# Optimization experiments

Measured on AMD Instinct MI355X. Metric: run time of the kernel, lower is better.

Reference implementation:

```python
import jax, jax.numpy as jnp
import numpy as np


def setup_inputs() -> dict:
    key = jax.random.key(0)
    k1, k2 = jax.random.split(key)
    x = jax.random.normal(k1, (16, 4096, 256), dtype=jnp.float32)
    embedding = jax.random.normal(k2, (1024, 256), dtype=jnp.float32)
    return {"x": x, "embedding": embedding}


def reference(x, embedding):
    # which_dim = -1 (default): no permute.
    shape = x.shape
    xf = x.reshape(-1, shape[-1])  # [N, D]
    x_sq = jnp.sum(xf * xf, axis=-1, keepdims=True)          # [N, 1]
    e_sq = jnp.sum(embedding * embedding, axis=-1)           # [K]
    dist = -(x_sq - 2.0 * (xf @ embedding.T) + e_sq[None, :])  # [N, K]
    embed_indices = jnp.argmax(dist, axis=1)                 # [N]
    embed_indices = embed_indices.reshape(shape[:-1])        # [B, S]
    quantization = embedding[embed_indices]                  # [B, S, D]
    return (quantization, embed_indices)
```

## Files before the change

kernel.cpp:

```cpp
#include <hip/hip_runtime.h>
#include <hip/hip_fp16.h>
#include <math.h>

#define MROWS   65536
#define NCODES  1024
#define KD      256
#define MARGIN  0.25f

typedef unsigned short u16;
typedef __attribute__((ext_vector_type(8))) _Float16 hfrag;
typedef __attribute__((ext_vector_type(4))) float f32x4;

#define IOFF ((size_t)MROWS * KD)

__device__ __forceinline__ float addrn(float a, float b) {
    float d; asm("v_add_f32 %0, %1, %2" : "=v"(d) : "v"(a), "v"(b)); return d;
}

__device__ __forceinline__ float sumsq_vf8ic4(const float* __restrict__ xr) {
    float a[4][8];
#pragma unroll
    for (int i = 0; i < 4; ++i)
#pragma unroll
        for (int l = 0; l < 8; ++l) a[i][l] = 0.f;
#pragma unroll
    for (int m = 0; m < 8; ++m)
#pragma unroll
        for (int i = 0; i < 4; ++i)
#pragma unroll
            for (int l = 0; l < 8; ++l) {
                float v = xr[m * 32 + i * 8 + l];
                a[i][l] = fmaf(v, v, a[i][l]);
            }
    float cc[8];
#pragma unroll
    for (int l = 0; l < 8; ++l)
        cc[l] = addrn(addrn(addrn(a[0][l], a[1][l]), a[2][l]), a[3][l]);
    float u0 = addrn(cc[0], cc[4]), u1 = addrn(cc[1], cc[5]);
    float u2 = addrn(cc[2], cc[6]), u3 = addrn(cc[3], cc[7]);
    return addrn(addrn(u0, u2), addrn(u1, u3));
}

__global__ __launch_bounds__(256)
void vq_pack(const float* __restrict__ src, u16* __restrict__ dh,
             unsigned int* __restrict__ cnt) {
    if (cnt && blockIdx.x == 0 && threadIdx.x == 0) *cnt = 0;
    __shared__ __align__(16) float lx[16 * 260];
    const int t = threadIdx.x;
    const size_t base = (size_t)blockIdx.x * 16 * 256;
#pragma unroll
    for (int qq = 0; qq < 4; ++qq) {
        int i4 = qq * 256 + t;
        int row = i4 >> 6, col = (i4 & 63) * 4;
        *(float4*)(lx + row * 260 + col) = *(const float4*)(src + base + (size_t)i4 * 4);
    }
    __syncthreads();
#pragma unroll
    for (int i = 0; i < 2; ++i) {
        int s = t + 256 * i;
        int kb = s >> 6, lane = s & 63;
        int r = lane & 15, kg = lane >> 4;
        int k0 = kb * 32 + kg * 8;
        u16 vh[8];
#pragma unroll
        for (int j = 0; j < 8; ++j) {
            float v = lx[r * 260 + k0 + j];
            vh[j] = __half_as_ushort(__float2half(v));
        }
        size_t off = (((size_t)blockIdx.x * 8 + kb) * 64 + lane) * 8;
        *(ulonglong2*)(dh + off) = *(ulonglong2*)vh;
    }
}

__global__ __launch_bounds__(256)
void vq_sumsq_llvm(const float* __restrict__ src, float* __restrict__ out) {
    __shared__ float lx[64 * 257];
    const int t = threadIdx.x;
    const size_t base = (size_t)blockIdx.x * 64 * 256;
#pragma unroll
    for (int qq = 0; qq < 16; ++qq) {
        int idx4 = qq * 256 + t;
        int row = idx4 >> 6, col4 = idx4 & 63;
        *(float4*)(lx + row * 257 + col4 * 4) = *(const float4*)(src + base + (size_t)idx4 * 4);
    }
    __syncthreads();
    if (t < 64) out[blockIdx.x * 64 + t] = sumsq_vf8ic4(lx + t * 257);
}

__global__ __launch_bounds__(256)
void vq_transpose(const float* __restrict__ emb, float* __restrict__ embT) {
    __shared__ float ld[64][65];
    const int t = threadIdx.x;
    const int c0 = blockIdx.x * 64, k0 = blockIdx.y * 64;
#pragma unroll
    for (int u = 0; u < 16; ++u) {
        int i = u * 256 + t;
        int r = i >> 6, col = i & 63;
        ld[r][col] = emb[(size_t)(c0 + r) * 256 + k0 + col];
    }
    __syncthreads();
#pragma unroll
    for (int u = 0; u < 16; ++u) {
        int i = u * 256 + t;
        int r = i >> 6, col = i & 63;
        embT[(size_t)(k0 + r) * 1024 + c0 + col] = ld[col][r];
    }
}

__global__ __launch_bounds__(256, 2)
void vq_gemm(const u16* __restrict__ Ah, const u16* __restrict__ Eh,
             const float* __restrict__ esq, float* __restrict__ tw) {
    extern __shared__ u16 ldsA[];
    const int t = threadIdx.x;
    const int wave = t >> 6, lane = t & 63;
    const int wm = wave >> 1, wn = wave & 1;
    const int q = lane >> 4, c = lane & 15;
    const int m0 = blockIdx.x * 128;
    const int mrb8 = blockIdx.x * 64;

#pragma unroll
    for (int u = 0; u < 16; ++u) {
        int f = wave * 16 + u;
        const u16* srcp = Ah + ((size_t)(mrb8 + f) * 64 + lane) * 8;
        __builtin_amdgcn_global_load_lds((const unsigned int*)srcp,
                                         (unsigned int*)(ldsA + f * 512), 16, 0, 0);
    }
    __syncthreads();

    auto LOADB = [&](int s, hfrag* dst) {
        const int f0 = ((s >> 3) * 64) + (wn * 4) * 8 + (s & 7);
#pragma unroll
        for (int ni = 0; ni < 4; ++ni)
            dst[ni] = *(const hfrag*)(Eh + (size_t)(f0 + ni * 8) * 512 + lane * 8);
    };
    auto LDA = [&](int s, hfrag* dst) {
        const int ks = s & 7;
#pragma unroll
        for (int mi = 0; mi < 4; ++mi)
            dst[mi] = *(const hfrag*)(ldsA + ((wm * 4 + mi) * 8 + ks) * 512 + lane * 8);
    };

    float b1[16], s2v[16], bi[16];
#pragma unroll
    for (int r = 0; r < 16; ++r) { b1[r] = INFINITY; s2v[r] = INFINITY; bi[r] = 0.f; }

    f32x4 acc[4][4];
#pragma unroll
    for (int mi = 0; mi < 4; ++mi)
#pragma unroll
        for (int ni = 0; ni < 4; ++ni) acc[mi][ni] = 0.f;

    hfrag bA[4], bB[4];
    LOADB(0, bA);
    LOADB(1, bB);

    for (int sp = 0; sp < 32; ++sp) {
        const int s0 = sp * 2, s1 = sp * 2 + 1;
        {
            hfrag nx[4];
            LOADB(s0 + 2 < 64 ? s0 + 2 : 0, nx);
            hfrag af[4];
            LDA(s0, af);
#pragma unroll
            for (int mi = 0; mi < 4; ++mi)
#pragma unroll
                for (int ni = 0; ni < 4; ++ni)
                    acc[mi][ni] = __builtin_amdgcn_mfma_f32_16x16x32_f16(af[mi], bA[ni], acc[mi][ni], 0, 0, 0);
#pragma unroll
            for (int ni = 0; ni < 4; ++ni) bA[ni] = nx[ni];
        }
        {
            hfrag nx[4];
            LOADB(s1 + 2 < 64 ? s1 + 2 : 0, nx);
            hfrag af[4];
            LDA(s1, af);
#pragma unroll
            for (int mi = 0; mi < 4; ++mi)
#pragma unroll
                for (int ni = 0; ni < 4; ++ni)
                    acc[mi][ni] = __builtin_amdgcn_mfma_f32_16x16x32_f16(af[mi], bB[ni], acc[mi][ni], 0, 0, 0);
#pragma unroll
            for (int ni = 0; ni < 4; ++ni) bB[ni] = nx[ni];
        }
        if ((s1 & 7) == 7) {
            const int nqi = s1 >> 3;
#pragma unroll
            for (int ni = 0; ni < 4; ++ni) {
                const int code = nqi * 128 + wn * 64 + ni * 16 + c;
                const float e2 = esq[code];
                const float ci = (float)code;
#pragma unroll
                for (int mi = 0; mi < 4; ++mi)
#pragma unroll
                    for (int j = 0; j < 4; ++j) {
                        const int r = mi * 4 + j;
                        float sc = fmaf(-2.f, acc[mi][ni][j], e2);
                        bool lt = sc < b1[r];
                        s2v[r] = fminf(s2v[r], lt ? b1[r] : sc);
                        if (lt) { b1[r] = sc; bi[r] = ci; }
                    }
            }
#pragma unroll
            for (int mi = 0; mi < 4; ++mi)
#pragma unroll
                for (int ni = 0; ni < 4; ++ni) acc[mi][ni] = 0.f;
        }
    }

#pragma unroll
    for (int r = 0; r < 16; ++r) {
#pragma unroll
        for (int mm = 1; mm < 16; mm <<= 1) {
            float ob = __shfl_xor(b1[r], mm, 64);
            float os = __shfl_xor(s2v[r], mm, 64);
            float oi = __shfl_xor(bi[r], mm, 64);
            if (ob < b1[r]) { s2v[r] = fminf(b1[r], os); b1[r] = ob; bi[r] = oi; }
            else            { s2v[r] = fminf(s2v[r], ob); }
        }
    }
    if (c == 0) {
#pragma unroll
        for (int mi = 0; mi < 4; ++mi)
#pragma unroll
            for (int j = 0; j < 4; ++j) {
                int row = m0 + wm * 64 + mi * 16 + q * 4 + j;
                size_t o = (size_t)row * 8 + wn * 4;
                int r = mi * 4 + j;
                tw[o + 0] = b1[r];
                tw[o + 1] = s2v[r];
                tw[o + 2] = bi[r];
            }
    }
}

__global__ void vq_reduce2(const float* __restrict__ tw, float* __restrict__ idxf,
                           unsigned int* __restrict__ cnt, int* __restrict__ list) {
    int row = blockIdx.x * 256 + threadIdx.x;
    float b0 = tw[(size_t)row * 8 + 0], s0 = tw[(size_t)row * 8 + 1], i0 = tw[(size_t)row * 8 + 2];
    float b1 = tw[(size_t)row * 8 + 4], s1 = tw[(size_t)row * 8 + 5], i1 = tw[(size_t)row * 8 + 6];
    float b, s2, bidx;
    if (b0 <= b1) { b = b0; bidx = i0; s2 = fminf(s0, b1); }
    else          { b = b1; bidx = i1; s2 = fminf(s1, b0); }
    idxf[row] = bidx;
    if (s2 - b < MARGIN) {
        unsigned int pos = atomicAdd(cnt, 1u);
        list[pos] = row;
    }
}

__global__ __launch_bounds__(256)
void vq_refine1(const float* __restrict__ x, const float* __restrict__ embT,
                const float* __restrict__ esq, const int* __restrict__ list,
                const unsigned int* __restrict__ cnt, float* __restrict__ idxf) {
    __shared__ __align__(16) float xs[8][260];
    __shared__ float xsq_s[8];
    __shared__ float lb[8][4];
    __shared__ int   li[8][4];
    const int t = threadIdx.x;
    const int wave = t >> 6, lane = t & 63;
    const unsigned int n = *cnt;
    float e2q[4];
#pragma unroll
    for (int qq = 0; qq < 4; ++qq) e2q[qq] = esq[qq * 256 + t];

    for (unsigned int g = blockIdx.x; g * 8u < n; g += gridDim.x) {
        const unsigned int r0 = g * 8u;
        const int nr = (int)min(8u, n - r0);
        __syncthreads();
#pragma unroll
        for (int u = 0; u < 2; ++u) {
            int s = u * 256 + t;
            int rr = s >> 6, l4 = s & 63;
            if (rr < nr) {
                int row = list[r0 + rr];
                *(float4*)(&xs[rr][l4 * 4]) = *(const float4*)(x + (size_t)row * 256 + l4 * 4);
            }
        }
        __syncthreads();
        if (t < nr) xsq_s[t] = sumsq_vf8ic4(&xs[t][0]);
        __syncthreads();

        float d[8][4];
#pragma unroll
        for (int r = 0; r < 8; ++r)
#pragma unroll
            for (int qq = 0; qq < 4; ++qq) d[r][qq] = 0.f;

        for (int kq = 0; kq < 64; ++kq) {
            float ev[4][4];
#pragma unroll
            for (int j = 0; j < 4; ++j)
#pragma unroll
                for (int qq = 0; qq < 4; ++qq)
                    ev[qq][j] = embT[(size_t)(kq * 4 + j) * 1024 + qq * 256 + t];
            float4 xf[8];
#pragma unroll
            for (int r = 0; r < 8; ++r) xf[r] = *(const float4*)(&xs[r][kq * 4]);
#pragma unroll
            for (int r = 0; r < 8; ++r)
#pragma unroll
                for (int qq = 0; qq < 4; ++qq) {
                    d[r][qq] = fmaf(xf[r].x, ev[qq][0], d[r][qq]);
                    d[r][qq] = fmaf(xf[r].y, ev[qq][1], d[r][qq]);
                    d[r][qq] = fmaf(xf[r].z, ev[qq][2], d[r][qq]);
                    d[r][qq] = fmaf(xf[r].w, ev[qq][3], d[r][qq]);
                }
        }
#pragma unroll
        for (int r = 0; r < 8; ++r) {
            float sv = INFINITY; int bc = 0x7fffffff;
#pragma unroll
            for (int qq = 0; qq < 4; ++qq) {
                float s = addrn(fmaf(-2.f, d[r][qq], xsq_s[r]), e2q[qq]);
                if (s < sv) { sv = s; bc = qq * 256 + t; }
            }
#pragma unroll
            for (int mm = 1; mm < 64; mm <<= 1) {
                float ob = __shfl_xor(sv, mm, 64);
                int oi = __shfl_xor(bc, mm, 64);
                if (ob < sv || (ob == sv && oi < bc)) { sv = ob; bc = oi; }
            }
            if (lane == 0) { lb[r][wave] = sv; li[r][wave] = bc; }
        }
        __syncthreads();
        if (t < nr) {
            float best = lb[t][0]; int bix = li[t][0];
#pragma unroll
            for (int w = 1; w < 4; ++w) {
                float ob = lb[t][w]; int oi = li[t][w];
                if (ob < best || (ob == best && oi < bix)) { best = ob; bix = oi; }
            }
            idxf[list[r0 + t]] = (float)bix;
        }
    }
}

__global__ void vq_gather(const float* __restrict__ emb, const float* __restrict__ idx_f,
                          float* __restrict__ qout) {
    int row = blockIdx.x * 4 + (threadIdx.x >> 6);
    int l = threadIdx.x & 63;
    int idx = (int)idx_f[row];
    float4 v = *(const float4*)(emb + (size_t)idx * KD + l * 4);
    *(float4*)(qout + (size_t)row * KD + l * 4) = v;
}

extern "C" void kernel_launch(void* const* d_in, const int* in_sizes, int n_in,
                              void* d_out, int out_size, void* d_ws, size_t ws_size,
                              hipStream_t stream) {
    const float* x   = (const float*)d_in[0];
    const float* emb = (const float*)d_in[1];
    float* out  = (float*)d_out;
    float* idxf = out + IOFF;

    u16* Ah = (u16*)out;
    float* embT = (float*)((char*)d_out + (32u << 20));

    char* ws = (char*)d_ws;
    u16* Eh    = (u16*)(ws);
    float* esq = (float*)(ws + (512 << 10));
    float* tw  = (float*)(ws + (1 << 20));
    unsigned int* cnt = (unsigned int*)(ws + ((size_t)3 << 20) + (512 << 10));
    int* list = (int*)(ws + ((size_t)3 << 20) + (512 << 10) + 256);

    vq_pack<<<dim3(MROWS / 16), dim3(256), 0, stream>>>(x, Ah, cnt);
    vq_pack<<<dim3(NCODES / 16), dim3(256), 0, stream>>>(emb, Eh, nullptr);
    vq_sumsq_llvm<<<dim3(NCODES / 64), dim3(256), 0, stream>>>(emb, esq);
    vq_transpose<<<dim3(16, 4), dim3(256), 0, stream>>>(emb, embT);
    vq_gemm<<<dim3(MROWS / 128), dim3(256), 65536, stream>>>(Ah, Eh, esq, tw);
    vq_reduce2<<<dim3(MROWS / 256), dim3(256), 0, stream>>>(tw, idxf, cnt, list);
    vq_refine1<<<dim3(512), dim3(256), 0, stream>>>(x, embT, esq, list, cnt, idxf);
    vq_gather<<<dim3(MROWS / 4), dim3(256), 0, stream>>>(emb, idxf, out);
}
```

Baseline: 138.8 us.

## Fuse embedding prep, in-block reduction and gather; widen GEMM to eight waves

Merges the three embedding preprocessing kernels (fp16 pack, squared norms, transpose) into one kernel that loads each tile once. The GEMM now runs 512 threads with a four-way code split, so each block covers 256 codes per pass in half as many steps. The per-row best and second-best across waves are combined in LDS, which removes the separate reduce kernel. The index write, flagging of ambiguous rows and quantization gather are fused into one kernel, and the refine kernel rewrites the gathered rows for the rows it fixes. This cuts launches and global round trips, but the launch bound of 512 threads with 4 blocks may squeeze registers and cause spills in the MFMA loop.

```diff
diff --git a/kernel.cpp b/kernel.cpp
--- a/kernel.cpp
+++ b/kernel.cpp
@@ -44,7 +44,7 @@
 __global__ __launch_bounds__(256)
 void vq_pack(const float* __restrict__ src, u16* __restrict__ dh,
              unsigned int* __restrict__ cnt) {
-    if (cnt && blockIdx.x == 0 && threadIdx.x == 0) *cnt = 0;
+    if (blockIdx.x == 0 && threadIdx.x == 0) *cnt = 0;
     __shared__ __align__(16) float lx[16 * 260];
     const int t = threadIdx.x;
     const size_t base = (size_t)blockIdx.x * 16 * 256;
@@ -73,54 +73,55 @@
 }
 
 __global__ __launch_bounds__(256)
-void vq_sumsq_llvm(const float* __restrict__ src, float* __restrict__ out) {
+void vq_prep_emb(const float* __restrict__ emb, u16* __restrict__ Eh,
+                 float* __restrict__ esq, float* __restrict__ embT) {
     __shared__ float lx[64 * 257];
     const int t = threadIdx.x;
-    const size_t base = (size_t)blockIdx.x * 64 * 256;
+    const int c0 = blockIdx.x * 64;
+    const size_t base = (size_t)c0 * 256;
 #pragma unroll
     for (int qq = 0; qq < 16; ++qq) {
         int idx4 = qq * 256 + t;
         int row = idx4 >> 6, col4 = idx4 & 63;
-        *(float4*)(lx + row * 257 + col4 * 4) = *(const float4*)(src + base + (size_t)idx4 * 4);
-    }
-    __syncthreads();
-    if (t < 64) out[blockIdx.x * 64 + t] = sumsq_vf8ic4(lx + t * 257);
-}
-
-__global__ __launch_bounds__(256)
-void vq_transpose(const float* __restrict__ emb, float* __restrict__ embT) {
-    __shared__ float ld[64][65];
-    const int t = threadIdx.x;
-    const int c0 = blockIdx.x * 64, k0 = blockIdx.y * 64;
-#pragma unroll
-    for (int u = 0; u < 16; ++u) {
-        int i = u * 256 + t;
-        int r = i >> 6, col = i & 63;
-        ld[r][col] = emb[(size_t)(c0 + r) * 256 + k0 + col];
-    }
-    __syncthreads();
-#pragma unroll
-    for (int u = 0; u < 16; ++u) {
-        int i = u * 256 + t;
-        int r = i >> 6, col = i & 63;
-        embT[(size_t)(k0 + r) * 1024 + c0 + col] = ld[col][r];
-    }
-}
-
-__global__ __launch_bounds__(256, 2)
+        *(float4*)(lx + row * 257 + col4 * 4) = *(const float4*)(emb + base + (size_t)idx4 * 4);
+    }
+    __syncthreads();
+    if (t < 64) esq[c0 + t] = sumsq_vf8ic4(lx + t * 257);
+#pragma unroll
+    for (int i = 0; i < 8; ++i) {
+        int s = i * 256 + t;
+        int fl = s >> 6, lane = s & 63;
+        int rb_l = fl >> 3, kb = fl & 7;
+        int r = rb_l * 16 + (lane & 15), kg = lane >> 4;
+        int k0 = kb * 32 + kg * 8;
+        u16 vh[8];
+#pragma unroll
+        for (int j = 0; j < 8; ++j)
+            vh[j] = __half_as_ushort(__float2half(lx[r * 257 + k0 + j]));
+        size_t off = (((size_t)(blockIdx.x * 4 + rb_l) * 8 + kb) * 64 + lane) * 8;
+        *(ulonglong2*)(Eh + off) = *(ulonglong2*)vh;
+    }
+#pragma unroll
+    for (int i = 0; i < 64; ++i) {
+        int k = i * 4 + (t >> 6), col = t & 63;
+        embT[(size_t)k * 1024 + c0 + col] = lx[col * 257 + k];
+    }
+}
+
+__global__ __launch_bounds__(512, 4)
 void vq_gemm(const u16* __restrict__ Ah, const u16* __restrict__ Eh,
              const float* __restrict__ esq, float* __restrict__ tw) {
     extern __shared__ u16 ldsA[];
     const int t = threadIdx.x;
     const int wave = t >> 6, lane = t & 63;
-    const int wm = wave >> 1, wn = wave & 1;
+    const int wm = wave >> 2, wn = wave & 3;
     const int q = lane >> 4, c = lane & 15;
     const int m0 = blockIdx.x * 128;
     const int mrb8 = blockIdx.x * 64;
 
 #pragma unroll
-    for (int u = 0; u < 16; ++u) {
-        int f = wave * 16 + u;
+    for (int u = 0; u < 8; ++u) {
+        int f = wave * 8 + u;
         const u16* srcp = Ah + ((size_t)(mrb8 + f) * 64 + lane) * 8;
         __builtin_amdgcn_global_load_lds((const unsigned int*)srcp,
                                          (unsigned int*)(ldsA + f * 512), 16, 0, 0);
@@ -128,7 +129,7 @@
     __syncthreads();
 
     auto LOADB = [&](int s, hfrag* dst) {
-        const int f0 = ((s >> 3) * 64) + (wn * 4) * 8 + (s & 7);
+        const int f0 = (s >> 3) * 128 + (wn * 4) * 8 + (s & 7);
 #pragma unroll
         for (int ni = 0; ni < 4; ++ni)
             dst[ni] = *(const hfrag*)(Eh + (size_t)(f0 + ni * 8) * 512 + lane * 8);
@@ -154,11 +155,11 @@
     LOADB(0, bA);
     LOADB(1, bB);
 
-    for (int sp = 0; sp < 32; ++sp) {
+    for (int sp = 0; sp < 16; ++sp) {
         const int s0 = sp * 2, s1 = sp * 2 + 1;
         {
             hfrag nx[4];
-            LOADB(s0 + 2 < 64 ? s0 + 2 : 0, nx);
+            LOADB(s0 + 2 < 32 ? s0 + 2 : 0, nx);
             hfrag af[4];
             LDA(s0, af);
 #pragma unroll
@@ -171,7 +172,7 @@
         }
         {
             hfrag nx[4];
-            LOADB(s1 + 2 < 64 ? s1 + 2 : 0, nx);
+            LOADB(s1 + 2 < 32 ? s1 + 2 : 0, nx);
             hfrag af[4];
             LDA(s1, af);
 #pragma unroll
@@ -183,10 +184,10 @@
             for (int ni = 0; ni < 4; ++ni) bB[ni] = nx[ni];
         }
         if ((s1 & 7) == 7) {
-            const int nqi = s1 >> 3;
+            const int p = s1 >> 3;
 #pragma unroll
             for (int ni = 0; ni < 4; ++ni) {
-                const int code = nqi * 128 + wn * 64 + ni * 16 + c;
+                const int code = p * 256 + wn * 64 + ni * 16 + c;
                 const float e2 = esq[code];
                 const float ci = (float)code;
 #pragma unroll
@@ -218,44 +219,78 @@
             else            { s2v[r] = fminf(s2v[r], ob); }
         }
     }
+    __syncthreads();
+    float* sm = (float*)ldsA;
     if (c == 0) {
 #pragma unroll
         for (int mi = 0; mi < 4; ++mi)
 #pragma unroll
             for (int j = 0; j < 4; ++j) {
-                int row = m0 + wm * 64 + mi * 16 + q * 4 + j;
-                size_t o = (size_t)row * 8 + wn * 4;
                 int r = mi * 4 + j;
-                tw[o + 0] = b1[r];
-                tw[o + 1] = s2v[r];
-                tw[o + 2] = bi[r];
-            }
-    }
-}
-
-__global__ void vq_reduce2(const float* __restrict__ tw, float* __restrict__ idxf,
-                           unsigned int* __restrict__ cnt, int* __restrict__ list) {
-    int row = blockIdx.x * 256 + threadIdx.x;
-    float b0 = tw[(size_t)row * 8 + 0], s0 = tw[(size_t)row * 8 + 1], i0 = tw[(size_t)row * 8 + 2];
-    float b1 = tw[(size_t)row * 8 + 4], s1 = tw[(size_t)row * 8 + 5], i1 = tw[(size_t)row * 8 + 6];
-    float b, s2, bidx;
-    if (b0 <= b1) { b = b0; bidx = i0; s2 = fminf(s0, b1); }
-    else          { b = b1; bidx = i1; s2 = fminf(s1, b0); }
-    idxf[row] = bidx;
-    if (s2 - b < MARGIN) {
-        unsigned int pos = atomicAdd(cnt, 1u);
-        list[pos] = row;
+                int row_l = wm * 64 + mi * 16 + q * 4 + j;
+                sm[row_l * 12 + wn * 3 + 0] = b1[r];
+                sm[row_l * 12 + wn * 3 + 1] = s2v[r];
+                sm[row_l * 12 + wn * 3 + 2] = bi[r];
+            }
+    }
+    __syncthreads();
+    if (t < 128) {
+        float b = INFINITY, s2 = INFINITY, bidx = 0.f;
+#pragma unroll
+        for (int w = 0; w < 4; ++w) {
+            float ob = sm[t * 12 + w * 3 + 0];
+            float os = sm[t * 12 + w * 3 + 1];
+            float oi = sm[t * 12 + w * 3 + 2];
+            if (ob < b) { s2 = fminf(b, os); b = ob; bidx = oi; }
+            else        { s2 = fminf(s2, ob); }
+        }
+        size_t row = (size_t)(m0 + t);
+        tw[row * 4 + 0] = b;
+        tw[row * 4 + 1] = s2;
+        tw[row * 4 + 2] = bidx;
     }
 }
 
 __global__ __launch_bounds__(256)
-void vq_refine1(const float* __restrict__ x, const float* __restrict__ embT,
-                const float* __restrict__ esq, const int* __restrict__ list,
-                const unsigned int* __restrict__ cnt, float* __restrict__ idxf) {
+void vq_flag_gather(const float* __restrict__ tw, const float* __restrict__ emb,
+                    float* __restrict__ idxf, float* __restrict__ quant,
+                    unsigned int* __restrict__ cnt, int* __restrict__ list) {
+    __shared__ int idx_l[64];
+    const int t = threadIdx.x;
+    const int r0 = blockIdx.x * 64;
+    if (t < 64) {
+        int row = r0 + t;
+        float b  = tw[(size_t)row * 4 + 0];
+        float s2 = tw[(size_t)row * 4 + 1];
+        int bidx = (int)tw[(size_t)row * 4 + 2];
+        idxf[row] = (float)bidx;
+        idx_l[t] = bidx;
+        if (s2 - b < MARGIN) {
+            unsigned int pos = atomicAdd(cnt, 1u);
+            list[pos] = row;
+        }
+    }
+    __syncthreads();
+    const int lane = t & 63, w = t >> 6;
+#pragma unroll
+    for (int u = 0; u < 16; ++u) {
+        int rl = u * 4 + w;
+        int idx = idx_l[rl];
+        *(float4*)(quant + (size_t)(r0 + rl) * 256 + lane * 4) =
+            *(const float4*)(emb + (size_t)idx * 256 + lane * 4);
+    }
+}
+
+__global__ __launch_bounds__(256)
+void vq_refine1(const float* __restrict__ x, const float* __restrict__ emb,
+                const float* __restrict__ embT, const float* __restrict__ esq,
+                const int* __restrict__ list, const unsigned int* __restrict__ cnt,
+                float* __restrict__ idxf, float* __restrict__ quant) {
     __shared__ __align__(16) float xs[8][260];
     __shared__ float xsq_s[8];
     __shared__ float lb[8][4];
     __shared__ int   li[8][4];
+    __shared__ int   li2[8];
     const int t = threadIdx.x;
     const int wave = t >> 6, lane = t & 63;
     const unsigned int n = *cnt;
@@ -331,17 +366,20 @@
                 if (ob < best || (ob == best && oi < bix)) { best = ob; bix = oi; }
             }
             idxf[list[r0 + t]] = (float)bix;
-        }
-    }
-}
-
-__global__ void vq_gather(const float* __restrict__ emb, const float* __restrict__ idx_f,
-                          float* __restrict__ qout) {
-    int row = blockIdx.x * 4 + (threadIdx.x >> 6);
-    int l = threadIdx.x & 63;
-    int idx = (int)idx_f[row];
-    float4 v = *(const float4*)(emb + (size_t)idx * KD + l * 4);
-    *(float4*)(qout + (size_t)row * KD + l * 4) = v;
+            li2[t] = bix;
+        }
+        __syncthreads();
+#pragma unroll
+        for (int rr = 0; rr < 2; ++rr) {
+            int rl = wave * 2 + rr;
+            if (rl < nr) {
+                int row = list[r0 + rl];
+                int idx = li2[rl];
+                *(float4*)(quant + (size_t)row * 256 + lane * 4) =
+                    *(const float4*)(emb + (size_t)idx * 256 + lane * 4);
+            }
+        }
+    }
 }
 
 extern "C" void kernel_launch(void* const* d_in, const int* in_sizes, int n_in,
@@ -353,21 +391,18 @@
     float* idxf = out + IOFF;
 
     u16* Ah = (u16*)out;
-    float* embT = (float*)((char*)d_out + (32u << 20));
 
     char* ws = (char*)d_ws;
     u16* Eh    = (u16*)(ws);
     float* esq = (float*)(ws + (512 << 10));
-    float* tw  = (float*)(ws + (1 << 20));
-    unsigned int* cnt = (unsigned int*)(ws + ((size_t)3 << 20) + (512 << 10));
-    int* list = (int*)(ws + ((size_t)3 << 20) + (512 << 10) + 256);
+    unsigned int* cnt = (unsigned int*)(ws + (640 << 10));
+    int* list  = (int*)(ws + (640 << 10) + 256);
+    float* embT = (float*)(ws + (1 << 20));
+    float* tw   = (float*)(ws + (2 << 20));
 
     vq_pack<<<dim3(MROWS / 16), dim3(256), 0, stream>>>(x, Ah, cnt);
-    vq_pack<<<dim3(NCODES / 16), dim3(256), 0, stream>>>(emb, Eh, nullptr);
-    vq_sumsq_llvm<<<dim3(NCODES / 64), dim3(256), 0, stream>>>(emb, esq);
-    vq_transpose<<<dim3(16, 4), dim3(256), 0, stream>>>(emb, embT);
-    vq_gemm<<<dim3(MROWS / 128), dim3(256), 65536, stream>>>(Ah, Eh, esq, tw);
-    vq_reduce2<<<dim3(MROWS / 256), dim3(256), 0, stream>>>(tw, idxf, cnt, list);
-    vq_refine1<<<dim3(512), dim3(256), 0, stream>>>(x, embT, esq, list, cnt, idxf);
-    vq_gather<<<dim3(MROWS / 4), dim3(256), 0, stream>>>(emb, idxf, out);
-}
+    vq_prep_emb<<<dim3(16), dim3(256), 0, stream>>>(emb, Eh, esq, embT);
+    vq_gemm<<<dim3(MROWS / 128), dim3(512), 65536, stream>>>(Ah, Eh, esq, tw);
+    vq_flag_gather<<<dim3(MROWS / 64), dim3(256), 0, stream>>>(tw, emb, idxf, out, cnt, list);
+    vq_refine1<<<dim3(512), dim3(256), 0, stream>>>(x, emb, embT, esq, list, cnt, idxf, out);
+}
```

New measurement: 206.1 us. 48.4% more time.
